# Kernel tuning notes

Measured on AMD Instinct MI355X. Metric: run time of the kernel, lower is better.

Reference implementation:

```python
import jax, jax.numpy as jnp
import numpy as np

LN_EPS = 1e-12  # config.layer_norm_eps (BERT default)


def setup_inputs() -> dict:
    key = jax.random.key(0)
    k1, k2, k3, k4 = jax.random.split(key, 4)
    B, S, D_IN, D_OUT = 16, 512, 4096, 1024
    return {
        "hidden_states": jax.random.normal(k1, (B, S, D_IN), dtype=jnp.float32),
        "input_tensor": jax.random.normal(k2, (B, S, D_OUT), dtype=jnp.float32),
        "W": jax.random.normal(k3, (D_OUT, D_IN), dtype=jnp.float32) * 0.02,
        "b": jax.random.normal(k4, (D_OUT,), dtype=jnp.float32) * 0.02,
        "gamma": jnp.ones((D_OUT,), dtype=jnp.float32),
        "beta": jnp.zeros((D_OUT,), dtype=jnp.float32),
    }


def reference(hidden_states, input_tensor, W, b, gamma, beta):
    # mix_Linear 1-bit path (XNOR-Net style): binarize weights with per-row scale
    alpha = jnp.mean(jnp.abs(W), axis=1, keepdims=True)   # [D_OUT, 1]
    W_q = jnp.sign(W) * alpha                              # [D_OUT, D_IN]
    # dense GEMM: [B,S,D_IN] x [D_OUT,D_IN]^T -> [B,S,D_OUT]
    h = jnp.einsum("bsi,oi->bso", hidden_states, W_q) + b
    # dropout is identity in eval mode; residual add + LayerNorm
    x = h + input_tensor
    mu = jnp.mean(x, axis=-1, keepdims=True)
    var = jnp.mean(jnp.square(x - mu), axis=-1, keepdims=True)
    return gamma * (x - mu) * jax.lax.rsqrt(var + LN_EPS) + beta
```

## Files before the change

### kernel.cpp

```cpp
#include <hip/hip_runtime.h>

using u16    = unsigned short;
using short8 = __attribute__((ext_vector_type(8))) short;
using u16x8  = __attribute__((ext_vector_type(8))) u16;
using u16x4  = __attribute__((ext_vector_type(4))) u16;
using f32x4  = __attribute__((ext_vector_type(4))) float;

#define M_DIM 8192
#define N_DIM 1024
#define K_DIM 4096

typedef __attribute__((address_space(1))) void gvoid;
typedef __attribute__((address_space(3))) void svoid;
#define GLOAD_LDS16(g, s) \
  __builtin_amdgcn_global_load_lds((gvoid*)(void*)(g), (svoid*)(s), 16, 0, 0)

__device__ __forceinline__ u16 f2bf(float f) {
  unsigned u = __builtin_bit_cast(unsigned, f);
  u = (u + 0x7FFFu + ((u >> 16) & 1u)) >> 16;
  return (u16)u;
}

__global__ __launch_bounds__(256) void wprep_kernel(const float* __restrict__ W,
                                                    u16* __restrict__ Wsgn,
                                                    float* __restrict__ alpha) {
  const int row = blockIdx.x;
  const int t   = threadIdx.x;
  const float4* wr = (const float4*)(W + (size_t)row * K_DIM);
  float4 v[4];
  float s = 0.f;
#pragma unroll
  for (int j = 0; j < 4; ++j) {
    v[j] = wr[t + 256 * j];
    s += fabsf(v[j].x) + fabsf(v[j].y) + fabsf(v[j].z) + fabsf(v[j].w);
  }
#pragma unroll
  for (int off = 32; off > 0; off >>= 1) s += __shfl_down(s, off, 64);
  __shared__ float red[4];
  if ((t & 63) == 0) red[t >> 6] = s;
  __syncthreads();
  if (t == 0) alpha[row] = (red[0] + red[1] + red[2] + red[3]) * (1.0f / K_DIM);
  u16x4* dst = (u16x4*)(Wsgn + (size_t)row * K_DIM);
#pragma unroll
  for (int j = 0; j < 4; ++j) {
    u16x4 sg;
    sg[0] = v[j].x > 0.f ? 0x3F80 : (v[j].x < 0.f ? 0xBF80 : 0);
    sg[1] = v[j].y > 0.f ? 0x3F80 : (v[j].y < 0.f ? 0xBF80 : 0);
    sg[2] = v[j].z > 0.f ? 0x3F80 : (v[j].z < 0.f ? 0xBF80 : 0);
    sg[3] = v[j].w > 0.f ? 0x3F80 : (v[j].w < 0.f ? 0xBF80 : 0);
    dst[t + 256 * j] = sg;
  }
}

__global__ __launch_bounds__(256) void cast_kernel(const float* __restrict__ in,
                                                   u16* __restrict__ out) {
  const size_t i = ((size_t)blockIdx.x * 256 + threadIdx.x) * 8;
  float4 a = ((const float4*)(in + i))[0];
  float4 b = ((const float4*)(in + i))[1];
  u16x8 p;
  p[0] = f2bf(a.x); p[1] = f2bf(a.y); p[2] = f2bf(a.z); p[3] = f2bf(a.w);
  p[4] = f2bf(b.x); p[5] = f2bf(b.y); p[6] = f2bf(b.z); p[7] = f2bf(b.w);
  *(u16x8*)(out + i) = p;
}

template <bool PRE>
__global__ __launch_bounds__(256) void gemm_kernel(const void* __restrict__ Aopaque,
                                                   const u16* __restrict__ Bsgn,
                                                   const float* __restrict__ alpha,
                                                   const float* __restrict__ bias,
                                                   const float* __restrict__ resid,
                                                   float* __restrict__ out) {
  __shared__ u16 lA[128 * 32];
  __shared__ u16 lB[128 * 32];
  const int tid  = threadIdx.x;
  const int wave = tid >> 6;
  const int lane = tid & 63;
  const int quad = lane >> 4;
  const int l16  = lane & 15;
  const int wm   = (wave >> 1) * 64;
  const int wn   = (wave & 1) * 64;
  const size_t m0 = (size_t)blockIdx.y * 128;
  const size_t n0 = (size_t)blockIdx.x * 128;

  f32x4 acc[4][4] = {};

  const int chunk = wave * 2;
  const int ld_r  = lane >> 2;
  const int ld_k  = (lane & 3) * 8;

  for (int k0 = 0; k0 < K_DIM; k0 += 32) {
    GLOAD_LDS16(Bsgn + (n0 + (size_t)(chunk)*16 + ld_r) * K_DIM + k0 + ld_k,
                lB + chunk * 512);
    GLOAD_LDS16(Bsgn + (n0 + (size_t)(chunk + 1)*16 + ld_r) * K_DIM + k0 + ld_k,
                lB + (chunk + 1) * 512);
    if constexpr (PRE) {
      const u16* A = (const u16*)Aopaque;
      GLOAD_LDS16(A + (m0 + (size_t)(chunk)*16 + ld_r) * K_DIM + k0 + ld_k,
                  lA + chunk * 512);
      GLOAD_LDS16(A + (m0 + (size_t)(chunk + 1)*16 + ld_r) * K_DIM + k0 + ld_k,
                  lA + (chunk + 1) * 512);
    } else {
      const float* A = (const float*)Aopaque;
      const int row = tid >> 1;
      const int ks  = (tid & 1) * 16;
      const float4* g = (const float4*)(A + (m0 + row) * (size_t)K_DIM + k0 + ks);
      float4 f0 = g[0], f1 = g[1], f2 = g[2], f3 = g[3];
      u16x8 p0, p1;
      p0[0] = f2bf(f0.x); p0[1] = f2bf(f0.y); p0[2] = f2bf(f0.z); p0[3] = f2bf(f0.w);
      p0[4] = f2bf(f1.x); p0[5] = f2bf(f1.y); p0[6] = f2bf(f1.z); p0[7] = f2bf(f1.w);
      p1[0] = f2bf(f2.x); p1[1] = f2bf(f2.y); p1[2] = f2bf(f2.z); p1[3] = f2bf(f2.w);
      p1[4] = f2bf(f3.x); p1[5] = f2bf(f3.y); p1[6] = f2bf(f3.z); p1[7] = f2bf(f3.w);
      *(u16x8*)(lA + row * 32 + ks)     = p0;
      *(u16x8*)(lA + row * 32 + ks + 8) = p1;
    }
    asm volatile("s_waitcnt vmcnt(0)" ::: "memory");
    __syncthreads();

    short8 af[4], bf[4];
#pragma unroll
    for (int mt = 0; mt < 4; ++mt)
      af[mt] = *(const short8*)(lA + (wm + mt * 16 + l16) * 32 + quad * 8);
#pragma unroll
    for (int nt = 0; nt < 4; ++nt)
      bf[nt] = *(const short8*)(lB + (wn + nt * 16 + l16) * 32 + quad * 8);
#pragma unroll
    for (int mt = 0; mt < 4; ++mt)
#pragma unroll
      for (int nt = 0; nt < 4; ++nt)
        acc[mt][nt] = __builtin_amdgcn_mfma_f32_16x16x32_bf16(af[mt], bf[nt],
                                                              acc[mt][nt], 0, 0, 0);
    __syncthreads();
  }

#pragma unroll
  for (int nt = 0; nt < 4; ++nt) {
    const size_t n  = n0 + wn + nt * 16 + l16;
    const float  al = alpha[n];
    const float  bi = bias[n];
#pragma unroll
    for (int mt = 0; mt < 4; ++mt) {
      const size_t mbase = m0 + wm + mt * 16 + quad * 4;
#pragma unroll
      for (int r = 0; r < 4; ++r) {
        const size_t mm = mbase + r;
        out[mm * N_DIM + n] = acc[mt][nt][r] * al + bi + resid[mm * N_DIM + n];
      }
    }
  }
}

__global__ __launch_bounds__(256) void ln_kernel(float* __restrict__ x,
                                                 const float* __restrict__ gamma,
                                                 const float* __restrict__ beta) {
  const size_t row = blockIdx.x;
  float4* xr = (float4*)(x + row * N_DIM);
  const int t = threadIdx.x;
  float4 v = xr[t];
  float s  = v.x + v.y + v.z + v.w;
  float sq = v.x * v.x + v.y * v.y + v.z * v.z + v.w * v.w;
#pragma unroll
  for (int off = 32; off > 0; off >>= 1) {
    s  += __shfl_down(s, off, 64);
    sq += __shfl_down(sq, off, 64);
  }
  __shared__ float rs[4], rq[4];
  if ((t & 63) == 0) { rs[t >> 6] = s; rq[t >> 6] = sq; }
  __syncthreads();
  s  = rs[0] + rs[1] + rs[2] + rs[3];
  sq = rq[0] + rq[1] + rq[2] + rq[3];
  const float mu  = s * (1.0f / N_DIM);
  float var = sq * (1.0f / N_DIM) - mu * mu;
  var = fmaxf(var, 0.0f);
  const float inv = rsqrtf(var + 1e-12f);
  const float4 g = ((const float4*)gamma)[t];
  const float4 b = ((const float4*)beta)[t];
  v.x = g.x * ((v.x - mu) * inv) + b.x;
  v.y = g.y * ((v.y - mu) * inv) + b.y;
  v.z = g.z * ((v.z - mu) * inv) + b.z;
  v.w = g.w * ((v.w - mu) * inv) + b.w;
  xr[t] = v;
}

extern "C" void kernel_launch(void* const* d_in, const int* in_sizes, int n_in,
                              void* d_out, int out_size, void* d_ws, size_t ws_size,
                              hipStream_t stream) {
  const float* hidden = (const float*)d_in[0];
  const float* resid  = (const float*)d_in[1];
  const float* W      = (const float*)d_in[2];
  const float* bias   = (const float*)d_in[3];
  const float* gamma  = (const float*)d_in[4];
  const float* beta   = (const float*)d_in[5];
  float* out = (float*)d_out;

  char* ws = (char*)d_ws;
  u16*   Wsgn  = (u16*)ws;
  float* alpha = (float*)(ws + 8ull * 1024 * 1024);
  u16*   Abf   = (u16*)(ws + 8ull * 1024 * 1024 + 4096);
  const size_t need_full = 8ull * 1024 * 1024 + 4096 + 64ull * 1024 * 1024;

  wprep_kernel<<<N_DIM, 256, 0, stream>>>(W, Wsgn, alpha);

  dim3 ggrid(N_DIM / 128, M_DIM / 128);
  if (ws_size >= need_full) {
    cast_kernel<<<(M_DIM * (size_t)K_DIM) / (256 * 8), 256, 0, stream>>>(hidden, Abf);
    gemm_kernel<true><<<ggrid, 256, 0, stream>>>((const void*)Abf, Wsgn, alpha,
                                                 bias, resid, out);
  } else {
    gemm_kernel<false><<<ggrid, 256, 0, stream>>>((const void*)hidden, Wsgn, alpha,
                                                  bias, resid, out);
  }
  ln_kernel<<<M_DIM, 256, 0, stream>>>(out, gamma, beta);
}
```

Before: 352.8 us.

## Swizzle LDS tiles with XOR and remap blocks for XCD-local L2 reuse

Applies an XOR swizzle to the 16-byte k-chunks in the LDS A and B tiles, both on the global_load_lds writes and on the MFMA fragment reads, to cut LDS bank conflicts. It also moves the GEMM to a 1D grid whose block index is remapped so that blocks on the same XCD (block id mod 8) share a contiguous band of M rows across all N tiles, aiming for better L2 reuse of the A tiles. Both changes must keep the write and read index maps consistent, and the remap assumes a fixed 8-XCD round-robin dispatch.

```diff
diff --git a/kernel.cpp b/kernel.cpp
--- a/kernel.cpp
+++ b/kernel.cpp
@@ -79,14 +79,18 @@
   const int l16  = lane & 15;
   const int wm   = (wave >> 1) * 64;
   const int wn   = (wave & 1) * 64;
-  const size_t m0 = (size_t)blockIdx.y * 128;
-  const size_t n0 = (size_t)blockIdx.x * 128;
+
+  const int b   = blockIdx.x;
+  const int xcd = b & 7;
+  const int l   = b >> 3;
+  const size_t m0 = (size_t)(xcd * 8 + (l >> 3)) * 128;
+  const size_t n0 = (size_t)(l & 7) * 128;
 
   f32x4 acc[4][4] = {};
 
   const int chunk = wave * 2;
   const int ld_r  = lane >> 2;
-  const int ld_k  = (lane & 3) * 8;
+  const int ld_k  = (((lane & 3) ^ (ld_r & 3)) * 8);
 
   for (int k0 = 0; k0 < K_DIM; k0 += 32) {
     GLOAD_LDS16(Bsgn + (n0 + (size_t)(chunk)*16 + ld_r) * K_DIM + k0 + ld_k,
@@ -102,27 +106,32 @@
     } else {
       const float* A = (const float*)Aopaque;
       const int row = tid >> 1;
-      const int ks  = (tid & 1) * 16;
-      const float4* g = (const float4*)(A + (m0 + row) * (size_t)K_DIM + k0 + ks);
+      const int g0  = (tid & 1) * 2;
+      const float4* g = (const float4*)(A + (m0 + row) * (size_t)K_DIM + k0 + g0 * 8);
       float4 f0 = g[0], f1 = g[1], f2 = g[2], f3 = g[3];
       u16x8 p0, p1;
       p0[0] = f2bf(f0.x); p0[1] = f2bf(f0.y); p0[2] = f2bf(f0.z); p0[3] = f2bf(f0.w);
       p0[4] = f2bf(f1.x); p0[5] = f2bf(f1.y); p0[6] = f2bf(f1.z); p0[7] = f2bf(f1.w);
       p1[0] = f2bf(f2.x); p1[1] = f2bf(f2.y); p1[2] = f2bf(f2.z); p1[3] = f2bf(f2.w);
       p1[4] = f2bf(f3.x); p1[5] = f2bf(f3.y); p1[6] = f2bf(f3.z); p1[7] = f2bf(f3.w);
-      *(u16x8*)(lA + row * 32 + ks)     = p0;
-      *(u16x8*)(lA + row * 32 + ks + 8) = p1;
+      const int base = (row >> 4) * 512 + (row & 15) * 32;
+      *(u16x8*)(lA + base + ((g0 ^ (row & 3)) * 8))       = p0;
+      *(u16x8*)(lA + base + (((g0 + 1) ^ (row & 3)) * 8)) = p1;
     }
     asm volatile("s_waitcnt vmcnt(0)" ::: "memory");
     __syncthreads();
 
     short8 af[4], bf[4];
 #pragma unroll
-    for (int mt = 0; mt < 4; ++mt)
-      af[mt] = *(const short8*)(lA + (wm + mt * 16 + l16) * 32 + quad * 8);
-#pragma unroll
-    for (int nt = 0; nt < 4; ++nt)
-      bf[nt] = *(const short8*)(lB + (wn + nt * 16 + l16) * 32 + quad * 8);
+    for (int mt = 0; mt < 4; ++mt) {
+      const int base = ((wm >> 4) + mt) * 512 + l16 * 32;
+      af[mt] = *(const short8*)(lA + base + ((quad ^ (l16 & 3)) * 8));
+    }
+#pragma unroll
+    for (int nt = 0; nt < 4; ++nt) {
+      const int base = ((wn >> 4) + nt) * 512 + l16 * 32;
+      bf[nt] = *(const short8*)(lB + base + ((quad ^ (l16 & 3)) * 8));
+    }
 #pragma unroll
     for (int mt = 0; mt < 4; ++mt)
 #pragma unroll
@@ -200,14 +209,14 @@
 
   wprep_kernel<<<N_DIM, 256, 0, stream>>>(W, Wsgn, alpha);
 
-  dim3 ggrid(N_DIM / 128, M_DIM / 128);
+  const int nblocks = (N_DIM / 128) * (M_DIM / 128);
   if (ws_size >= need_full) {
     cast_kernel<<<(M_DIM * (size_t)K_DIM) / (256 * 8), 256, 0, stream>>>(hidden, Abf);
-    gemm_kernel<true><<<ggrid, 256, 0, stream>>>((const void*)Abf, Wsgn, alpha,
-                                                 bias, resid, out);
+    gemm_kernel<true><<<nblocks, 256, 0, stream>>>((const void*)Abf, Wsgn, alpha,
+                                                   bias, resid, out);
   } else {
-    gemm_kernel<false><<<ggrid, 256, 0, stream>>>((const void*)hidden, Wsgn, alpha,
-                                                  bias, resid, out);
+    gemm_kernel<false><<<nblocks, 256, 0, stream>>>((const void*)hidden, Wsgn, alpha,
+                                                    bias, resid, out);
   }
   ln_kernel<<<M_DIM, 256, 0, stream>>>(out, gamma, beta);
 }
```

New measurement: 344.3 us. 1.02x faster.

## Fuse fp32-to-bf16 cast into GEMM with 64x128 tiles, XCD swizzle and LDS XOR swizzle

Applied to the files above, without the earlier changes.

Removes the separate cast kernel and the bf16 copy of the activations, always converting fp32 A inside the GEMM load path. The block tile shrinks from 128x128 to 64x128 with a launch-bounds occupancy hint, a 1D grid remapped so that each XCD gets contiguous M tiles, and XOR swizzling of LDS columns to reduce bank conflicts. In exchange, the fp32 A is read once per N tile (8 times) instead of bf16, and each MFMA has less per-tile reuse, while the cast's extra write and read pass over 64MB disappears.

```diff
diff --git a/kernel.cpp b/kernel.cpp
--- a/kernel.cpp
+++ b/kernel.cpp
@@ -52,79 +52,67 @@
   }
 }
 
-__global__ __launch_bounds__(256) void cast_kernel(const float* __restrict__ in,
-                                                   u16* __restrict__ out) {
-  const size_t i = ((size_t)blockIdx.x * 256 + threadIdx.x) * 8;
-  float4 a = ((const float4*)(in + i))[0];
-  float4 b = ((const float4*)(in + i))[1];
-  u16x8 p;
-  p[0] = f2bf(a.x); p[1] = f2bf(a.y); p[2] = f2bf(a.z); p[3] = f2bf(a.w);
-  p[4] = f2bf(b.x); p[5] = f2bf(b.y); p[6] = f2bf(b.z); p[7] = f2bf(b.w);
-  *(u16x8*)(out + i) = p;
-}
-
-template <bool PRE>
-__global__ __launch_bounds__(256) void gemm_kernel(const void* __restrict__ Aopaque,
-                                                   const u16* __restrict__ Bsgn,
-                                                   const float* __restrict__ alpha,
-                                                   const float* __restrict__ bias,
-                                                   const float* __restrict__ resid,
-                                                   float* __restrict__ out) {
-  __shared__ u16 lA[128 * 32];
+__global__ __launch_bounds__(256, 4) void gemm_kernel(const float* __restrict__ A,
+                                                      const u16* __restrict__ Bsgn,
+                                                      const float* __restrict__ alpha,
+                                                      const float* __restrict__ bias,
+                                                      const float* __restrict__ resid,
+                                                      float* __restrict__ out) {
+  __shared__ u16 lA[64 * 32];
   __shared__ u16 lB[128 * 32];
   const int tid  = threadIdx.x;
   const int wave = tid >> 6;
   const int lane = tid & 63;
   const int quad = lane >> 4;
   const int l16  = lane & 15;
-  const int wm   = (wave >> 1) * 64;
+  const int wm   = (wave >> 1) * 32;
   const int wn   = (wave & 1) * 64;
-  const size_t m0 = (size_t)blockIdx.y * 128;
-  const size_t n0 = (size_t)blockIdx.x * 128;
 
-  f32x4 acc[4][4] = {};
+  const int b    = blockIdx.x;
+  const int xcd  = b & 7;
+  const int l    = b >> 3;
+  const size_t m0 = (size_t)(xcd * 16 + (l >> 3)) * 64;
+  const size_t n0 = (size_t)(l & 7) * 128;
 
-  const int chunk = wave * 2;
-  const int ld_r  = lane >> 2;
-  const int ld_k  = (lane & 3) * 8;
+  f32x4 acc[2][4] = {};
+
+  const int b_r = lane >> 2;
+  const int b_k = (((lane & 3) ^ (b_r & 3)) * 8);
+  const u16* bsrc0 = Bsgn + (n0 + (size_t)wave * 32 + b_r) * K_DIM + b_k;
+  const u16* bsrc1 = Bsgn + (n0 + (size_t)wave * 32 + 16 + b_r) * K_DIM + b_k;
+  u16* bdst0 = lB + wave * 1024;
+  u16* bdst1 = lB + wave * 1024 + 512;
+
+  const int a_r = tid >> 2;
+  const int a_g = tid & 3;
+  const float* asrc = A + (m0 + a_r) * (size_t)K_DIM + a_g * 8;
+  u16* adst = lA + a_r * 32 + ((a_g ^ (a_r & 3)) * 8);
 
   for (int k0 = 0; k0 < K_DIM; k0 += 32) {
-    GLOAD_LDS16(Bsgn + (n0 + (size_t)(chunk)*16 + ld_r) * K_DIM + k0 + ld_k,
-                lB + chunk * 512);
-    GLOAD_LDS16(Bsgn + (n0 + (size_t)(chunk + 1)*16 + ld_r) * K_DIM + k0 + ld_k,
-                lB + (chunk + 1) * 512);
-    if constexpr (PRE) {
-      const u16* A = (const u16*)Aopaque;
-      GLOAD_LDS16(A + (m0 + (size_t)(chunk)*16 + ld_r) * K_DIM + k0 + ld_k,
-                  lA + chunk * 512);
-      GLOAD_LDS16(A + (m0 + (size_t)(chunk + 1)*16 + ld_r) * K_DIM + k0 + ld_k,
-                  lA + (chunk + 1) * 512);
-    } else {
-      const float* A = (const float*)Aopaque;
-      const int row = tid >> 1;
-      const int ks  = (tid & 1) * 16;
-      const float4* g = (const float4*)(A + (m0 + row) * (size_t)K_DIM + k0 + ks);
-      float4 f0 = g[0], f1 = g[1], f2 = g[2], f3 = g[3];
-      u16x8 p0, p1;
-      p0[0] = f2bf(f0.x); p0[1] = f2bf(f0.y); p0[2] = f2bf(f0.z); p0[3] = f2bf(f0.w);
-      p0[4] = f2bf(f1.x); p0[5] = f2bf(f1.y); p0[6] = f2bf(f1.z); p0[7] = f2bf(f1.w);
-      p1[0] = f2bf(f2.x); p1[1] = f2bf(f2.y); p1[2] = f2bf(f2.z); p1[3] = f2bf(f2.w);
-      p1[4] = f2bf(f3.x); p1[5] = f2bf(f3.y); p1[6] = f2bf(f3.z); p1[7] = f2bf(f3.w);
-      *(u16x8*)(lA + row * 32 + ks)     = p0;
-      *(u16x8*)(lA + row * 32 + ks + 8) = p1;
-    }
+    GLOAD_LDS16(bsrc0 + k0, bdst0);
+    GLOAD_LDS16(bsrc1 + k0, bdst1);
+    float4 f0 = ((const float4*)(asrc + k0))[0];
+    float4 f1 = ((const float4*)(asrc + k0))[1];
+    u16x8 p;
+    p[0] = f2bf(f0.x); p[1] = f2bf(f0.y); p[2] = f2bf(f0.z); p[3] = f2bf(f0.w);
+    p[4] = f2bf(f1.x); p[5] = f2bf(f1.y); p[6] = f2bf(f1.z); p[7] = f2bf(f1.w);
+    *(u16x8*)adst = p;
     asm volatile("s_waitcnt vmcnt(0)" ::: "memory");
     __syncthreads();
 
-    short8 af[4], bf[4];
+    short8 af[2], bf[4];
 #pragma unroll
-    for (int mt = 0; mt < 4; ++mt)
-      af[mt] = *(const short8*)(lA + (wm + mt * 16 + l16) * 32 + quad * 8);
+    for (int mt = 0; mt < 2; ++mt) {
+      const int row = wm + mt * 16 + l16;
+      af[mt] = *(const short8*)(lA + row * 32 + ((quad ^ (l16 & 3)) * 8));
+    }
 #pragma unroll
-    for (int nt = 0; nt < 4; ++nt)
-      bf[nt] = *(const short8*)(lB + (wn + nt * 16 + l16) * 32 + quad * 8);
+    for (int nt = 0; nt < 4; ++nt) {
+      const int col = wn + nt * 16 + l16;
+      bf[nt] = *(const short8*)(lB + col * 32 + ((quad ^ (l16 & 3)) * 8));
+    }
 #pragma unroll
-    for (int mt = 0; mt < 4; ++mt)
+    for (int mt = 0; mt < 2; ++mt)
 #pragma unroll
       for (int nt = 0; nt < 4; ++nt)
         acc[mt][nt] = __builtin_amdgcn_mfma_f32_16x16x32_bf16(af[mt], bf[nt],
@@ -138,7 +126,7 @@
     const float  al = alpha[n];
     const float  bi = bias[n];
 #pragma unroll
-    for (int mt = 0; mt < 4; ++mt) {
+    for (int mt = 0; mt < 2; ++mt) {
       const size_t mbase = m0 + wm + mt * 16 + quad * 4;
 #pragma unroll
       for (int r = 0; r < 4; ++r) {
@@ -195,19 +183,11 @@
   char* ws = (char*)d_ws;
   u16*   Wsgn  = (u16*)ws;
   float* alpha = (float*)(ws + 8ull * 1024 * 1024);
-  u16*   Abf   = (u16*)(ws + 8ull * 1024 * 1024 + 4096);
-  const size_t need_full = 8ull * 1024 * 1024 + 4096 + 64ull * 1024 * 1024;
 
   wprep_kernel<<<N_DIM, 256, 0, stream>>>(W, Wsgn, alpha);
 
-  dim3 ggrid(N_DIM / 128, M_DIM / 128);
-  if (ws_size >= need_full) {
-    cast_kernel<<<(M_DIM * (size_t)K_DIM) / (256 * 8), 256, 0, stream>>>(hidden, Abf);
-    gemm_kernel<true><<<ggrid, 256, 0, stream>>>((const void*)Abf, Wsgn, alpha,
-                                                 bias, resid, out);
-  } else {
-    gemm_kernel<false><<<ggrid, 256, 0, stream>>>((const void*)hidden, Wsgn, alpha,
-                                                  bias, resid, out);
-  }
+  const int nblocks = (M_DIM / 64) * (N_DIM / 128);
+  gemm_kernel<<<nblocks, 256, 0, stream>>>(hidden, Wsgn, alpha, bias, resid, out);
+
   ln_kernel<<<M_DIM, 256, 0, stream>>>(out, gamma, beta);
 }
```

Result: slower. 403.7 us (+14.4%).
